# Optimization experiments

Hardware: AMD Instinct MI355X
Metric: run time of the kernel (lower is better)

## Reference

```python
import jax, jax.numpy as jnp
import numpy as np

M, N, D = 2048, 131072, 256

def setup_inputs() -> dict:
    key = jax.random.key(0)
    kq, kv = jax.random.split(key)
    query = jax.random.normal(kq, (M, D), dtype=jnp.float32)
    vectors = jax.random.normal(kv, (N, D), dtype=jnp.float32)
    return {"query": query, "vectors": vectors}

def reference(query, vectors):
    # torch.cdist(query, vectors, p=2).argmin(dim=1)
    # Euclidean distance via ||q||^2 + ||v||^2 - 2 q.v (GEMM-based, same math)
    q_sq = jnp.sum(query * query, axis=-1, keepdims=True)        # [M,1]
    v_sq = jnp.sum(vectors * vectors, axis=-1)                    # [N]
    cross = jnp.einsum('md,nd->mn', query, vectors)               # [M,N]
    dist_sq = jnp.maximum(q_sq + v_sq[None, :] - 2.0 * cross, 0.0)
    # sqrt is monotonic so argmin(dist) == argmin(dist_sq); take sqrt for faithfulness
    dist = jnp.sqrt(dist_sq)
    return jnp.argmin(dist, axis=1)                               # [M] int
```

## Files before the change

kernel.cpp:

```cpp
#include <hip/hip_runtime.h>
#include <hip/hip_bf16.h>

#define M 2048
#define N 131072
#define D 256

#define SLICE_G 64
#define NSLICE  (N / (SLICE_G * 16))
#define BIAS    1024.0f

typedef __attribute__((ext_vector_type(8))) _Float16 half8;
typedef __attribute__((ext_vector_type(8))) short short8;
typedef __attribute__((ext_vector_type(4))) float f32x4;
typedef unsigned long long ull;

__device__ __forceinline__ ull pack_key(float score, unsigned idx) {
    unsigned u = __float_as_uint(score);
    u = (u & 0x80000000u) ? ~u : (u | 0x80000000u);
    return ((ull)u << 32) | idx;
}

__device__ __forceinline__ void gload_lds16(const void* g, void* l) {
    __builtin_amdgcn_global_load_lds(
        (const __attribute__((address_space(1))) void*)g,
        (__attribute__((address_space(3))) void*)l, 16, 0, 0);
}

__global__ __launch_bounds__(256) void convert_fused(const float* __restrict__ v,
                                                     const float* __restrict__ q,
                                                     short* __restrict__ vf,
                                                     short* __restrict__ qf,
                                                     float* __restrict__ vsqb,
                                                     ull* __restrict__ keys) {
    __shared__ float part[4][16];

    const int b    = blockIdx.x;
    const bool isV = (b < N / 16);
    const int g    = isV ? b : (b - N / 16);
    const float* x = isV ? v : q;
    short* xf      = isV ? vf : qf;

    const int t    = threadIdx.x;
    const int w    = t >> 6;
    const int l    = t & 63;
    const int quad = (l >> 4) & 3;
    const int tx   = l & 15;

    const float* src = x + (size_t)g * 4096;
    float s = 0.f;
#pragma unroll
    for (int h = 0; h < 2; ++h) {
        const int c = w + h * 4;
        const float* p = src + tx * 256 + c * 32 + quad * 8;
        const float4 f0 = *(const float4*)p;
        const float4 f1 = *(const float4*)(p + 4);
        float tmp[8] __attribute__((aligned(16))) = {f0.x, f0.y, f0.z, f0.w,
                                                     f1.x, f1.y, f1.z, f1.w};
        half8 hh;
#pragma unroll
        for (int e = 0; e < 8; ++e) {
            hh[e] = (_Float16)tmp[e];
            s += tmp[e] * tmp[e];
        }
        *(short8*)(xf + ((size_t)g * 8 + c) * 512 + l * 8) = *(short8*)&hh;
    }

    if (isV) {
        s += __shfl_xor(s, 16, 64);
        s += __shfl_xor(s, 32, 64);
        if (l < 16) part[w][l] = s;
        __syncthreads();
        if (t < 16) vsqb[g * 16 + t] = part[0][t] + part[1][t] + part[2][t] + part[3][t] + BIAS;
    } else if (g == 0) {
        for (int i = t; i < 2 * M; i += 256) keys[i] = ~0ull;
    }
}

__global__ __launch_bounds__(256, 2) void dist_argmin_reg(const short* __restrict__ qf,
                                                          const short* __restrict__ vf,
                                                          const float* __restrict__ vsqb,
                                                          ull* __restrict__ keys1,
                                                          ull* __restrict__ keys2) {
    __shared__ short bt[2][8 * 512];

    const int tid  = threadIdx.x;
    const int lane = tid & 63;
    const int w    = tid >> 6;
    const int tx   = lane & 15;
    const int quad = (lane >> 4) & 3;

    const int lb    = blockIdx.x;
    const int xcd   = lb & 7;
    const int s_    = lb >> 3;
    const int slice = xcd * 16 + (s_ >> 3);
    const int qblk  = s_ & 7;

    const int qb0 = qblk * 256 + w * 64;
    const int sg0 = slice * SLICE_G;

    half8 aq[4][8];
#pragma unroll
    for (int mt = 0; mt < 4; ++mt)
#pragma unroll
        for (int c = 0; c < 8; ++c)
            aq[mt][c] = *(const half8*)(qf + ((size_t)((qb0 >> 4) + mt) * 8 + c) * 512 + lane * 8);

    unsigned best[16];
#pragma unroll
    for (int i = 0; i < 16; ++i) best[i] = 0xFFFFFFFFu;

    const short* bslice = vf + (size_t)sg0 * 8 * 512;
    const float* vp     = vsqb + sg0 * 16 + tx;

    auto stage = [&](short* buf, int g) {
        const short* gsrc = bslice + (size_t)g * 4096;
#pragma unroll
        for (int i = 0; i < 2; ++i) {
            const int seg = w * 2 + i;
            gload_lds16(gsrc + seg * 512 + lane * 8, buf + seg * 512);
        }
    };

    auto compute = [&](const short* buf, int g) {
        const float vsqr = vp[(size_t)g * 16];
        f32x4 acc[4];
#pragma unroll
        for (int i = 0; i < 4; ++i) acc[i] = (f32x4){0.f, 0.f, 0.f, 0.f};
#pragma unroll
        for (int c = 0; c < 8; ++c) {
            const half8 bfr = *(const half8*)(buf + c * 512 + lane * 8);
#pragma unroll
            for (int mt = 0; mt < 4; ++mt)
                acc[mt] = __builtin_amdgcn_mfma_f32_16x16x32_f16(aq[mt][c], bfr, acc[mt], 0, 0, 0);
        }
#pragma unroll
        for (int mt = 0; mt < 4; ++mt)
#pragma unroll
            for (int r = 0; r < 4; ++r) {
                const float sc = fmaf(-2.f, acc[mt][r], vsqr);
                const unsigned key = (__float_as_uint(sc) & 0xFFFFFFC0u) | (unsigned)g;
                const int sl = mt * 4 + r;
                best[sl] = key < best[sl] ? key : best[sl];
            }
    };

    stage(bt[0], 0);
    __syncthreads();

    for (int g = 0; g < SLICE_G; g += 2) {
        stage(bt[1], g + 1);
        compute(bt[0], g);
        __syncthreads();
        if (g + 2 < SLICE_G) stage(bt[0], g + 2);
        compute(bt[1], g + 1);
        __syncthreads();
    }

#pragma unroll
    for (int mt = 0; mt < 4; ++mt)
#pragma unroll
        for (int r = 0; r < 4; ++r) {
            const int sl = mt * 4 + r;
            unsigned k = best[sl];
#pragma unroll
            for (int off = 8; off; off >>= 1) {
                const unsigned o = (unsigned)__shfl_xor((int)k, off, 16);
                k = o < k ? o : k;
            }
            const ull bal = __ballot(best[sl] == k);
            const unsigned grp = (unsigned)((bal >> (quad * 16)) & 0xFFFFull);
            const int wtx = __ffs((int)grp) - 1;
            const unsigned n = (unsigned)((sg0 + (int)(k & 63u)) * 16 + wtx);
            if (tx == 0) {
                const int row = qb0 + mt * 16 + quad * 4 + r;
                const ull key64 = ((ull)k << 32) | n;
                const ull old = atomicMin(&keys1[row], key64);
                const ull loser = (key64 < old) ? old : key64;
                if (loser != ~0ull) atomicMin(&keys2[row], loser);
            }
        }
}

__global__ __launch_bounds__(256) void rescore_kernel(const float* __restrict__ q,
                                                      const float* __restrict__ v,
                                                      const ull* __restrict__ keys1,
                                                      const ull* __restrict__ keys2,
                                                      int* __restrict__ out) {
    const int qi   = blockIdx.x * 4 + (threadIdx.x >> 6);
    const int lane = threadIdx.x & 63;
    const float4 qv = *(const float4*)(q + (size_t)qi * D + lane * 4);
    ull best = ~0ull;
    ull cand[2];
    cand[0] = keys1[qi];
    cand[1] = keys2[qi];
#pragma unroll
    for (int c = 0; c < 2; ++c) {
        if (cand[c] == ~0ull) continue;
        const unsigned idx = (unsigned)cand[c];
        const float4 vv = *(const float4*)(v + (size_t)idx * D + lane * 4);
        float s1 = vv.x * vv.x + vv.y * vv.y + vv.z * vv.z + vv.w * vv.w;
        float s2 = qv.x * vv.x + qv.y * vv.y + qv.z * vv.z + qv.w * vv.w;
#pragma unroll
        for (int off = 32; off; off >>= 1) {
            s1 += __shfl_xor(s1, off, 64);
            s2 += __shfl_xor(s2, off, 64);
        }
        const float dist = fmaf(-2.0f, s2, s1);
        const ull key = pack_key(dist, idx);
        best = best < key ? best : key;
    }
    if (lane == 0) out[qi] = (int)(unsigned)(best & 0xFFFFFFFFull);
}

extern "C" void kernel_launch(void* const* d_in, const int* in_sizes, int n_in,
                              void* d_out, int out_size, void* d_ws, size_t ws_size,
                              hipStream_t stream) {
    const float* q = (const float*)d_in[0];
    const float* v = (const float*)d_in[1];
    int* out = (int*)d_out;

    char* ws = (char*)d_ws;
    float* vsqb = (float*)ws;                ws += (size_t)N * sizeof(float);
    ull* keys1 = (ull*)ws;                   ws += (size_t)2 * M * sizeof(ull);
    ull* keys2 = keys1 + M;
    short* qf = (short*)ws;                  ws += (size_t)M * D * 2;
    short* vf = (short*)ws;

    convert_fused<<<N / 16 + M / 16, 256, 0, stream>>>(v, q, vf, qf, vsqb, keys1);

    dist_argmin_reg<<<(M / 256) * NSLICE, 256, 0, stream>>>(qf, vf, vsqb, keys1, keys2);

    rescore_kernel<<<M / 4, 256, 0, stream>>>(q, v, keys1, keys2, out);
}
```

Measured before the change: 326.3 us.

## Fuse vector fp16 conversion and norm computation into distance kernel

After: 427.9 us. 31.1% more time.

```diff
diff --git a/kernel.cpp b/kernel.cpp
--- a/kernel.cpp
+++ b/kernel.cpp
@@ -26,62 +26,39 @@
         (__attribute__((address_space(3))) void*)l, 16, 0, 0);
 }
 
-__global__ __launch_bounds__(256) void convert_fused(const float* __restrict__ v,
-                                                     const float* __restrict__ q,
-                                                     short* __restrict__ vf,
-                                                     short* __restrict__ qf,
-                                                     float* __restrict__ vsqb,
-                                                     ull* __restrict__ keys) {
-    __shared__ float part[4][16];
-
-    const int b    = blockIdx.x;
-    const bool isV = (b < N / 16);
-    const int g    = isV ? b : (b - N / 16);
-    const float* x = isV ? v : q;
-    short* xf      = isV ? vf : qf;
-
+__global__ __launch_bounds__(256) void q_convert(const float* __restrict__ q,
+                                                 short* __restrict__ qf,
+                                                 ull* __restrict__ keys) {
+    const int g    = blockIdx.x;
     const int t    = threadIdx.x;
     const int w    = t >> 6;
     const int l    = t & 63;
     const int quad = (l >> 4) & 3;
     const int tx   = l & 15;
 
-    const float* src = x + (size_t)g * 4096;
-    float s = 0.f;
+    const float* src = q + (size_t)g * 4096;
 #pragma unroll
     for (int h = 0; h < 2; ++h) {
         const int c = w + h * 4;
         const float* p = src + tx * 256 + c * 32 + quad * 8;
         const float4 f0 = *(const float4*)p;
         const float4 f1 = *(const float4*)(p + 4);
-        float tmp[8] __attribute__((aligned(16))) = {f0.x, f0.y, f0.z, f0.w,
-                                                     f1.x, f1.y, f1.z, f1.w};
         half8 hh;
-#pragma unroll
-        for (int e = 0; e < 8; ++e) {
-            hh[e] = (_Float16)tmp[e];
-            s += tmp[e] * tmp[e];
-        }
-        *(short8*)(xf + ((size_t)g * 8 + c) * 512 + l * 8) = *(short8*)&hh;
+        hh[0] = (_Float16)f0.x; hh[1] = (_Float16)f0.y;
+        hh[2] = (_Float16)f0.z; hh[3] = (_Float16)f0.w;
+        hh[4] = (_Float16)f1.x; hh[5] = (_Float16)f1.y;
+        hh[6] = (_Float16)f1.z; hh[7] = (_Float16)f1.w;
+        *(short8*)(qf + ((size_t)g * 8 + c) * 512 + l * 8) = *(short8*)&hh;
     }
-
-    if (isV) {
-        s += __shfl_xor(s, 16, 64);
-        s += __shfl_xor(s, 32, 64);
-        if (l < 16) part[w][l] = s;
-        __syncthreads();
-        if (t < 16) vsqb[g * 16 + t] = part[0][t] + part[1][t] + part[2][t] + part[3][t] + BIAS;
-    } else if (g == 0) {
+    if (g == 0)
         for (int i = t; i < 2 * M; i += 256) keys[i] = ~0ull;
-    }
-}
-
-__global__ __launch_bounds__(256, 2) void dist_argmin_reg(const short* __restrict__ qf,
-                                                          const short* __restrict__ vf,
-                                                          const float* __restrict__ vsqb,
-                                                          ull* __restrict__ keys1,
-                                                          ull* __restrict__ keys2) {
-    __shared__ short bt[2][8 * 512];
+}
+
+__global__ __launch_bounds__(256, 2) void dist_argmin_fused(const short* __restrict__ qf,
+                                                            const float* __restrict__ v,
+                                                            ull* __restrict__ keys1,
+                                                            ull* __restrict__ keys2) {
+    __shared__ float bt[2][16 * 256];
 
     const int tid  = threadIdx.x;
     const int lane = tid & 63;
@@ -109,30 +86,44 @@
 #pragma unroll
     for (int i = 0; i < 16; ++i) best[i] = 0xFFFFFFFFu;
 
-    const short* bslice = vf + (size_t)sg0 * 8 * 512;
-    const float* vp     = vsqb + sg0 * 16 + tx;
-
-    auto stage = [&](short* buf, int g) {
-        const short* gsrc = bslice + (size_t)g * 4096;
-#pragma unroll
-        for (int i = 0; i < 2; ++i) {
-            const int seg = w * 2 + i;
-            gload_lds16(gsrc + seg * 512 + lane * 8, buf + seg * 512);
+    const float* vbase = v + (size_t)sg0 * 16 * 256;
+
+    auto stage = [&](float* buf, int g) {
+        const float* gsrc = vbase + (size_t)g * 4096;
+#pragma unroll
+        for (int i = 0; i < 4; ++i) {
+            const int row = w * 4 + i;
+            gload_lds16(gsrc + row * 256 + ((lane ^ (row & 7)) << 2), buf + row * 256);
         }
     };
 
-    auto compute = [&](const short* buf, int g) {
-        const float vsqr = vp[(size_t)g * 16];
+    auto compute = [&](const float* buf, int g) {
         f32x4 acc[4];
 #pragma unroll
         for (int i = 0; i < 4; ++i) acc[i] = (f32x4){0.f, 0.f, 0.f, 0.f};
+        float vs0 = 0.f, vs1 = 0.f, vs2 = 0.f, vs3 = 0.f;
 #pragma unroll
         for (int c = 0; c < 8; ++c) {
-            const half8 bfr = *(const half8*)(buf + c * 512 + lane * 8);
+            const int gc = c * 8 + quad * 2;
+            const float4 f0 = *(const float4*)&buf[tx * 256 + ((gc ^ (tx & 7)) << 2)];
+            const float4 f1 = *(const float4*)&buf[tx * 256 + (((gc + 1) ^ (tx & 7)) << 2)];
+            vs0 = fmaf(f0.x, f0.x, vs0); vs1 = fmaf(f0.y, f0.y, vs1);
+            vs2 = fmaf(f0.z, f0.z, vs2); vs3 = fmaf(f0.w, f0.w, vs3);
+            vs0 = fmaf(f1.x, f1.x, vs0); vs1 = fmaf(f1.y, f1.y, vs1);
+            vs2 = fmaf(f1.z, f1.z, vs2); vs3 = fmaf(f1.w, f1.w, vs3);
+            half8 b;
+            b[0] = (_Float16)f0.x; b[1] = (_Float16)f0.y;
+            b[2] = (_Float16)f0.z; b[3] = (_Float16)f0.w;
+            b[4] = (_Float16)f1.x; b[5] = (_Float16)f1.y;
+            b[6] = (_Float16)f1.z; b[7] = (_Float16)f1.w;
 #pragma unroll
             for (int mt = 0; mt < 4; ++mt)
-                acc[mt] = __builtin_amdgcn_mfma_f32_16x16x32_f16(aq[mt][c], bfr, acc[mt], 0, 0, 0);
-        }
+                acc[mt] = __builtin_amdgcn_mfma_f32_16x16x32_f16(aq[mt][c], b, acc[mt], 0, 0, 0);
+        }
+        float vs = (vs0 + vs1) + (vs2 + vs3);
+        vs += __shfl_xor(vs, 16, 64);
+        vs += __shfl_xor(vs, 32, 64);
+        const float vsqr = vs + BIAS;
 #pragma unroll
         for (int mt = 0; mt < 4; ++mt)
 #pragma unroll
@@ -220,15 +211,13 @@
     int* out = (int*)d_out;
 
     char* ws = (char*)d_ws;
-    float* vsqb = (float*)ws;                ws += (size_t)N * sizeof(float);
     ull* keys1 = (ull*)ws;                   ws += (size_t)2 * M * sizeof(ull);
     ull* keys2 = keys1 + M;
-    short* qf = (short*)ws;                  ws += (size_t)M * D * 2;
-    short* vf = (short*)ws;
-
-    convert_fused<<<N / 16 + M / 16, 256, 0, stream>>>(v, q, vf, qf, vsqb, keys1);
-
-    dist_argmin_reg<<<(M / 256) * NSLICE, 256, 0, stream>>>(qf, vf, vsqb, keys1, keys2);
+    short* qf = (short*)ws;
+
+    q_convert<<<M / 16, 256, 0, stream>>>(q, qf, keys1);
+
+    dist_argmin_fused<<<(M / 256) * NSLICE, 256, 0, stream>>>(qf, v, keys1, keys2);
 
     rescore_kernel<<<M / 4, 256, 0, stream>>>(q, v, keys1, keys2, out);
 }
```

## Stage four vector groups per barrier and use nontemporal loads in conversion

Applied to the files above, without the earlier changes.

Result: faster. 311.0 us (-4.7%).

```diff
diff --git a/kernel.cpp b/kernel.cpp
--- a/kernel.cpp
+++ b/kernel.cpp
@@ -1,5 +1,4 @@
 #include <hip/hip_runtime.h>
-#include <hip/hip_bf16.h>
 
 #define M 2048
 #define N 131072
@@ -7,6 +6,8 @@
 
 #define SLICE_G 64
 #define NSLICE  (N / (SLICE_G * 16))
+#define GEN     4
+#define NGEN    (SLICE_G / GEN)
 #define BIAS    1024.0f
 
 typedef __attribute__((ext_vector_type(8))) _Float16 half8;
@@ -30,8 +31,7 @@
                                                      const float* __restrict__ q,
                                                      short* __restrict__ vf,
                                                      short* __restrict__ qf,
-                                                     float* __restrict__ vsqb,
-                                                     ull* __restrict__ keys) {
+                                                     float* __restrict__ vsqb) {
     __shared__ float part[4][16];
 
     const int b    = blockIdx.x;
@@ -52,15 +52,15 @@
     for (int h = 0; h < 2; ++h) {
         const int c = w + h * 4;
         const float* p = src + tx * 256 + c * 32 + quad * 8;
-        const float4 f0 = *(const float4*)p;
-        const float4 f1 = *(const float4*)(p + 4);
-        float tmp[8] __attribute__((aligned(16))) = {f0.x, f0.y, f0.z, f0.w,
-                                                     f1.x, f1.y, f1.z, f1.w};
+        const f32x4 f0 = __builtin_nontemporal_load((const f32x4*)p);
+        const f32x4 f1 = __builtin_nontemporal_load((const f32x4*)p + 1);
         half8 hh;
 #pragma unroll
-        for (int e = 0; e < 8; ++e) {
-            hh[e] = (_Float16)tmp[e];
-            s += tmp[e] * tmp[e];
+        for (int e = 0; e < 4; ++e) {
+            hh[e]     = (_Float16)f0[e];
+            hh[e + 4] = (_Float16)f1[e];
+            s = fmaf(f0[e], f0[e], s);
+            s = fmaf(f1[e], f1[e], s);
         }
         *(short8*)(xf + ((size_t)g * 8 + c) * 512 + l * 8) = *(short8*)&hh;
     }
@@ -71,17 +71,15 @@
         if (l < 16) part[w][l] = s;
         __syncthreads();
         if (t < 16) vsqb[g * 16 + t] = part[0][t] + part[1][t] + part[2][t] + part[3][t] + BIAS;
-    } else if (g == 0) {
-        for (int i = t; i < 2 * M; i += 256) keys[i] = ~0ull;
-    }
-}
-
-__global__ __launch_bounds__(256, 2) void dist_argmin_reg(const short* __restrict__ qf,
+    }
+}
+
+__global__ __launch_bounds__(256, 2) void dist_argmin_lds(const short* __restrict__ qf,
                                                           const short* __restrict__ vf,
                                                           const float* __restrict__ vsqb,
                                                           ull* __restrict__ keys1,
                                                           ull* __restrict__ keys2) {
-    __shared__ short bt[2][8 * 512];
+    __shared__ short bt[2][GEN][8 * 512];
 
     const int tid  = threadIdx.x;
     const int lane = tid & 63;
@@ -109,30 +107,35 @@
 #pragma unroll
     for (int i = 0; i < 16; ++i) best[i] = 0xFFFFFFFFu;
 
-    const short* bslice = vf + (size_t)sg0 * 8 * 512;
-    const float* vp     = vsqb + sg0 * 16 + tx;
-
-    auto stage = [&](short* buf, int g) {
-        const short* gsrc = bslice + (size_t)g * 4096;
-#pragma unroll
-        for (int i = 0; i < 2; ++i) {
-            const int seg = w * 2 + i;
-            gload_lds16(gsrc + seg * 512 + lane * 8, buf + seg * 512);
+    const short* bsl = vf + (size_t)sg0 * 8 * 512;
+    const float* vp  = vsqb + sg0 * 16 + tx;
+
+    auto stage = [&](int buf, int gbase) {
+#pragma unroll
+        for (int t = 0; t < GEN; ++t) {
+            const short* gs = bsl + (size_t)(gbase + t) * 4096;
+#pragma unroll
+            for (int i = 0; i < 2; ++i) {
+                const int c = w + i * 4;
+                gload_lds16(gs + c * 512 + lane * 8, &bt[buf][t][c * 512]);
+            }
         }
     };
 
-    auto compute = [&](const short* buf, int g) {
+    auto compute = [&](int buf, int t, int g) {
         const float vsqr = vp[(size_t)g * 16];
         f32x4 acc[4];
 #pragma unroll
         for (int i = 0; i < 4; ++i) acc[i] = (f32x4){0.f, 0.f, 0.f, 0.f};
+        __builtin_amdgcn_s_setprio(1);
 #pragma unroll
         for (int c = 0; c < 8; ++c) {
-            const half8 bfr = *(const half8*)(buf + c * 512 + lane * 8);
+            const half8 b = *(const half8*)&bt[buf][t][c * 512 + lane * 8];
 #pragma unroll
             for (int mt = 0; mt < 4; ++mt)
-                acc[mt] = __builtin_amdgcn_mfma_f32_16x16x32_f16(aq[mt][c], bfr, acc[mt], 0, 0, 0);
-        }
+                acc[mt] = __builtin_amdgcn_mfma_f32_16x16x32_f16(aq[mt][c], b, acc[mt], 0, 0, 0);
+        }
+        __builtin_amdgcn_s_setprio(0);
 #pragma unroll
         for (int mt = 0; mt < 4; ++mt)
 #pragma unroll
@@ -144,16 +147,16 @@
             }
     };
 
-    stage(bt[0], 0);
+    stage(0, 0);
     __syncthreads();
 
-    for (int g = 0; g < SLICE_G; g += 2) {
-        stage(bt[1], g + 1);
-        compute(bt[0], g);
+    int buf = 0;
+    for (int gen = 0; gen < NGEN; ++gen) {
+        if (gen + 1 < NGEN) stage(buf ^ 1, (gen + 1) * GEN);
+#pragma unroll
+        for (int t = 0; t < GEN; ++t) compute(buf, t, gen * GEN + t);
         __syncthreads();
-        if (g + 2 < SLICE_G) stage(bt[0], g + 2);
-        compute(bt[1], g + 1);
-        __syncthreads();
+        buf ^= 1;
     }
 
 #pragma unroll
@@ -220,15 +223,17 @@
     int* out = (int*)d_out;
 
     char* ws = (char*)d_ws;
-    float* vsqb = (float*)ws;                ws += (size_t)N * sizeof(float);
     ull* keys1 = (ull*)ws;                   ws += (size_t)2 * M * sizeof(ull);
     ull* keys2 = keys1 + M;
+    float* vsqb = (float*)ws;                ws += (size_t)N * sizeof(float);
     short* qf = (short*)ws;                  ws += (size_t)M * D * 2;
     short* vf = (short*)ws;
 
-    convert_fused<<<N / 16 + M / 16, 256, 0, stream>>>(v, q, vf, qf, vsqb, keys1);
-
-    dist_argmin_reg<<<(M / 256) * NSLICE, 256, 0, stream>>>(qf, vf, vsqb, keys1, keys2);
+    hipMemsetAsync(keys1, 0xFF, (size_t)2 * M * sizeof(ull), stream);
+
+    convert_fused<<<N / 16 + M / 16, 256, 0, stream>>>(v, q, vf, qf, vsqb);
+
+    dist_argmin_lds<<<(M / 256) * NSLICE, 256, 0, stream>>>(qf, vf, vsqb, keys1, keys2);
 
     rescore_kernel<<<M / 4, 256, 0, stream>>>(q, v, keys1, keys2, out);
 }
```
